# Performance work log

Measured on AMD Instinct MI355X. Metric: run time of the kernel, lower is better.

Reference implementation:

```python
import jax, jax.numpy as jnp
import numpy as np
from jax import lax

B, T = 1024, 1000
EPS = 1e-3  # keras BatchNormalization default epsilon
ALPHA = 0.2  # tf.nn.leaky_relu default alpha


def setup_inputs() -> dict:
    key = jax.random.key(0)
    ks = jax.random.split(key, 40)
    f32 = jnp.float32
    n = lambda k, s, sc=0.1: jax.random.normal(k, s, dtype=f32) * sc
    inp = {"x": jax.random.normal(ks[0], (B, 2, T, 1), dtype=f32)}
    # main conv stack (HWIO kernels)
    inp["c1k"] = n(ks[1], (1, 5, 1, 10));  inp["c1b"] = n(ks[2], (10,), 0.01)
    inp["c2k"] = n(ks[3], (1, 5, 10, 10)); inp["c2b"] = n(ks[4], (10,), 0.01)
    inp["c3k"] = n(ks[5], (1, 5, 10, 10)); inp["c3b"] = n(ks[6], (10,), 0.01)
    inp["c4k"] = n(ks[7], (2, 1, 10, 20)); inp["c4b"] = n(ks[8], (20,), 0.01)
    # batchnorm (inference) params
    for i, k0 in zip((1, 2, 3), (9, 13, 17)):
        inp[f"g{i}"]  = 1.0 + n(ks[k0], (10,), 0.05)
        inp[f"be{i}"] = n(ks[k0 + 1], (10,), 0.05)
        inp[f"m{i}"]  = n(ks[k0 + 2], (10,), 0.05)
        inp[f"v{i}"]  = 1.0 + jax.random.uniform(ks[k0 + 3], (10,), dtype=f32) * 0.1
    # dense head: flatten of [B,1,T-12,20]
    inp["dns_w"] = n(ks[21], ((T - 12) * 20, 1), 0.02)
    inp["dns_b"] = jnp.zeros((1,), f32)
    # MHRSSA blocks: 10 heads of Conv2D(2,(2,1)) stacked -> K [10,2,Cin,2], b [10,2];
    # depthwise (1,5) over 10 channels -> dw [5,10], db [10]
    inp["a1K"] = n(ks[22], (10, 2, 1, 2));  inp["a1b"] = n(ks[23], (10, 2), 0.01)
    inp["a1dw"] = n(ks[24], (5, 10));       inp["a1db"] = n(ks[25], (10,), 0.01)
    inp["a2K"] = n(ks[26], (10, 2, 10, 2)); inp["a2b"] = n(ks[27], (10, 2), 0.01)
    inp["a2dw"] = n(ks[28], (5, 10));       inp["a2db"] = n(ks[29], (10,), 0.01)
    inp["a3K"] = n(ks[30], (10, 2, 10, 2)); inp["a3b"] = n(ks[31], (10, 2), 0.01)
    inp["a3dw"] = n(ks[32], (5, 10));       inp["a3db"] = n(ks[33], (10,), 0.01)
    return inp


def conv2d(x, k, b):
    return lax.conv_general_dilated(x, k, (1, 1), 'VALID',
                                    dimension_numbers=('NHWC', 'HWIO', 'NHWC')) + b


def bn_inf(x, g, be, m, v):
    return (x - m) * (g * lax.rsqrt(v + EPS)) + be


def lrelu(x):
    return jnp.where(x >= 0, x, ALPHA * x)


def mhrssa(x, K, b, dw, db):
    # x: [B,2,T,C]; K: [10,2,C,2] (10 heads of a (2,1)-valid conv) -> [B,10,T,2]
    m = jnp.einsum('bhtc,ihco->bito', x, K) + b[None, :, None, :]
    a = jnp.transpose(m, (0, 3, 2, 1))  # [B,2,T,10]
    Tt = a.shape[2]
    # depthwise (1,5) valid conv over time, per-channel taps dw[w,i]
    y = sum(a[:, :, w:w + Tt - 4, :] * dw[w] for w in range(5)) + db
    return jax.nn.softmax(y, axis=-1)


def reference(x, c1k, c1b, g1, be1, m1, v1, c2k, c2b, g2, be2, m2, v2,
              c3k, c3b, g3, be3, m3, v3, c4k, c4b, dns_w, dns_b,
              a1K, a1b, a1dw, a1db, a2K, a2b, a2dw, a2db, a3K, a3b, a3dw, a3db):
    att1 = mhrssa(x, a1K, a1b, a1dw, a1db)
    h = lrelu(bn_inf(conv2d(x, c1k, c1b), g1, be1, m1, v1)) * att1
    att2 = mhrssa(h, a2K, a2b, a2dw, a2db)
    h = lrelu(bn_inf(conv2d(h, c2k, c2b), g2, be2, m2, v2)) * att2
    att3 = mhrssa(h, a3K, a3b, a3dw, a3db)
    h = lrelu(bn_inf(conv2d(h, c3k, c3b), g3, be3, m3, v3)) * att3
    h = lrelu(conv2d(h, c4k, c4b))          # [B,1,T-12,20]
    h = h.reshape(h.shape[0], -1)
    return h @ dns_w + dns_b                # RGS mode: raw scalar output
```

## Files before the change

### kernel.cpp

```cpp
#include <hip/hip_runtime.h>

#define REP10(X) X(0) X(1) X(2) X(3) X(4) X(5) X(6) X(7) X(8) X(9)
#define REP5(X)  X(0) X(1) X(2) X(3) X(4)

typedef __attribute__((ext_vector_type(2))) float v2;

#define SMX 136

__device__ __forceinline__ void fold_stage(
    float* dst, const float* g, const float* be, const float* mn,
    const float* vr, const float* cb, const float* adw, const float* adb,
    const float* aK, const float* ab, int CIN)
{
  const int tid = threadIdx.x;
  if (tid < 10) {
    const float sc = g[tid] * rsqrtf(vr[tid] + 1e-3f);
    dst[tid]      = sc;
    dst[10 + tid] = (cb[tid] - mn[tid]) * sc + be[tid];
    dst[70 + tid] = adb[tid] * 1.44269504088896340736f;
  }
  if (tid >= 10 && tid < 60)
    dst[10 + tid] = adw[tid - 10] * 1.44269504088896340736f;
  if (tid < 20)
    dst[80 + tid] = ab[(tid % 10) * 2 + tid / 10];
  const int n = 2 * CIN * 2 * 10;
  for (int idx = tid; idx < n; idx += 64) {
    const int i  = idx % 10;
    const int r  = idx / 10;
    const int o  = r % 2;
    const int r2 = r / 2;
    const int ci = r2 % CIN;
    const int h  = r2 / CIN;
    dst[100 + idx] = aK[((i * 2 + h) * CIN + ci) * 2 + o];
  }
}

__global__ void prep_kernel(
    const float* g1, const float* be1, const float* m1, const float* v1,
    const float* cb1, const float* a1dw, const float* a1db,
    const float* a1K, const float* a1b,
    const float* g2, const float* be2, const float* m2, const float* v2_,
    const float* cb2, const float* a2dw, const float* a2db,
    const float* a2K, const float* a2b,
    const float* g3, const float* be3, const float* m3, const float* v3,
    const float* cb3, const float* a3dw, const float* a3db,
    const float* a3K, const float* a3b,
    float* consts)
{
  fold_stage(consts,        g1, be1, m1, v1,  cb1, a1dw, a1db, a1K, a1b, 1);
  fold_stage(consts + 512,  g2, be2, m2, v2_, cb2, a2dw, a2db, a2K, a2b, 10);
  fold_stage(consts + 1024, g3, be3, m3, v3,  cb3, a3dw, a3db, a3K, a3b, 10);
}

template <int CIN>
__global__ __launch_bounds__(128) void stage_kernel(
    const float* __restrict__ in, float* __restrict__ outp, int Tout,
    const float* __restrict__ ck, const float* __restrict__ cst)
{
  __shared__ float smm[5 * SMX * 2];
  const int tid = threadIdx.x;
  const int o   = blockIdx.y;
  const int t0  = blockIdx.x * 128;
  const int Tin = Tout + 4;
  const float* __restrict__ inb =
      in + (size_t)blockIdx.z * (CIN == 1 ? 2000 : 20000);

  const float* __restrict__ scale  = cst;
  const float* __restrict__ shift2 = cst + 10;
  const float* __restrict__ adw2   = cst + 20;
  const float* __restrict__ adb2   = cst + 70;
  const float* __restrict__ abp    = cst + 80;
  const float* __restrict__ aKp    = cst + 100;

  for (int lt = tid; lt < 132; lt += 128) {
    const int t = t0 + lt;
    if (t < Tin) {
#define DECLM(p) v2 mp##p = *reinterpret_cast<const v2*>(abp + o * 10 + 2 * p);
      REP5(DECLM)
#undef DECLM
      if constexpr (CIN == 1) {
#pragma unroll
        for (int h = 0; h < 2; ++h) {
          const float xin = inb[h * 1000 + t];
          const v2 xs = {xin, xin};
          const float* kb = aKp + (h * 2 + o) * 10;
#define FMAM(p) mp##p = __builtin_elementwise_fma(                             \
              xs, *reinterpret_cast<const v2*>(kb + 2 * p), mp##p);
          REP5(FMAM)
#undef FMAM
        }
      } else {
#pragma unroll
        for (int h = 0; h < 2; ++h)
#pragma unroll
          for (int pc = 0; pc < 5; ++pc) {
            const v2 xv = *reinterpret_cast<const v2*>(
                inb + ((pc * 2 + h) * 1000 + t) * 2);
            const v2 xs0 = {xv.x, xv.x};
            const v2 xs1 = {xv.y, xv.y};
            const float* kb0 = aKp + ((h * CIN + 2 * pc) * 2 + o) * 10;
            const float* kb1 = aKp + ((h * CIN + 2 * pc + 1) * 2 + o) * 10;
#define FMAM(p) mp##p = __builtin_elementwise_fma(                             \
                xs0, *reinterpret_cast<const v2*>(kb0 + 2 * p), mp##p);        \
            mp##p = __builtin_elementwise_fma(                                 \
                xs1, *reinterpret_cast<const v2*>(kb1 + 2 * p), mp##p);
            REP5(FMAM)
#undef FMAM
          }
      }
#define STM(p) *reinterpret_cast<v2*>(&smm[(p * SMX + lt) * 2]) = mp##p;
      REP5(STM)
#undef STM
    }
  }
  __syncthreads();

  const int tt = t0 + tid;
  if (tt >= Tout) return;

#define DECLY(p) v2 yp##p = *reinterpret_cast<const v2*>(adb2 + 2 * p);
  REP5(DECLY)
#undef DECLY
#pragma unroll
  for (int w = 0; w < 5; ++w) {
    const float* aw = adw2 + w * 10;
#define FMAY(p) { const v2 sv =                                                \
        *reinterpret_cast<const v2*>(&smm[(p * SMX + tid + w) * 2]);           \
      yp##p = __builtin_elementwise_fma(                                       \
          sv, *reinterpret_cast<const v2*>(aw + 2 * p), yp##p); }
    REP5(FMAY)
#undef FMAY
  }

#define DECLA(p) v2 ap##p = {0.f, 0.f};
  REP5(DECLA)
#undef DECLA
  if constexpr (CIN == 1) {
    const float* __restrict__ cinb = inb + o * 1000 + tt;
#pragma unroll
    for (int w = 0; w < 5; ++w) {
      const float xin = cinb[w];
      const v2 xs = {xin, xin};
      const float* kb = ck + w * 10;
#define FMAC(p) ap##p = __builtin_elementwise_fma(                             \
          xs, *reinterpret_cast<const v2*>(kb + 2 * p), ap##p);
      REP5(FMAC)
#undef FMAC
    }
  } else {
#pragma unroll
    for (int w = 0; w < 5; ++w)
#pragma unroll
      for (int pc = 0; pc < 5; ++pc) {
        const v2 xv = *reinterpret_cast<const v2*>(
            inb + ((pc * 2 + o) * 1000 + tt + w) * 2);
        const v2 xs0 = {xv.x, xv.x};
        const v2 xs1 = {xv.y, xv.y};
        const float* kb0 = ck + (w * CIN + 2 * pc) * 10;
        const float* kb1 = ck + (w * CIN + 2 * pc + 1) * 10;
#define FMAC(p) ap##p = __builtin_elementwise_fma(                             \
            xs0, *reinterpret_cast<const v2*>(kb0 + 2 * p), ap##p);            \
        ap##p = __builtin_elementwise_fma(                                     \
            xs1, *reinterpret_cast<const v2*>(kb1 + 2 * p), ap##p);
        REP5(FMAC)
#undef FMAC
      }
  }

  const float y0 = yp0.x, y1 = yp0.y, y2 = yp1.x, y3 = yp1.y, y4 = yp2.x,
              y5 = yp2.y, y6 = yp3.x, y7 = yp3.y, y8 = yp4.x, y9 = yp4.y;
  float mx = y0;
  mx = fmaxf(mx, y1); mx = fmaxf(mx, y2); mx = fmaxf(mx, y3);
  mx = fmaxf(mx, y4); mx = fmaxf(mx, y5); mx = fmaxf(mx, y6);
  mx = fmaxf(mx, y7); mx = fmaxf(mx, y8); mx = fmaxf(mx, y9);
#define DECLE(i) const float e##i = exp2f(y##i - mx);
  REP10(DECLE)
#undef DECLE
  const float sm  = e0 + e1 + e2 + e3 + e4 + e5 + e6 + e7 + e8 + e9;
  const float inv = __builtin_amdgcn_rcpf(sm);

  float* __restrict__ ob =
      outp + (size_t)blockIdx.z * 20000 + (o * 1000 + tt) * 2;
#define STO(p, ea, eb) {                                                       \
    v2 bv = __builtin_elementwise_fma(                                         \
        ap##p, *reinterpret_cast<const v2*>(scale + 2 * p),                    \
        *reinterpret_cast<const v2*>(shift2 + 2 * p));                         \
    bv = __builtin_elementwise_max(bv, 0.2f * bv);                             \
    const v2 ev = {ea * inv, eb * inv};                                        \
    *reinterpret_cast<v2*>(ob + p * 4000) = bv * ev; }
  STO(0, e0, e1) STO(1, e2, e3) STO(2, e4, e5) STO(3, e6, e7) STO(4, e8, e9)
#undef STO
}

__global__ __launch_bounds__(256) void final_kernel(
    const float* __restrict__ h3, const float* __restrict__ c4k,
    const float* __restrict__ c4b, const float* __restrict__ dnsw,
    const float* __restrict__ dnsb, float* __restrict__ outp, int b0)
{
  __shared__ float red[4];
  const int tid = threadIdx.x;
  const float* __restrict__ hb = h3 + (size_t)blockIdx.x * 20000;
  v2 dotv = {0.f, 0.f};
#pragma unroll 1
  for (int t = tid; t < 988; t += 256) {
#define LDX(p)                                                                 \
    const v2 xa##p = *reinterpret_cast<const v2*>(hb + ((p*2+0)*1000 + t)*2);  \
    const v2 xc##p = *reinterpret_cast<const v2*>(hb + ((p*2+1)*1000 + t)*2);
    REP5(LDX)
#undef LDX
    const float* __restrict__ dwp = dnsw + t * 20;
#pragma unroll
    for (int q = 0; q < 10; ++q) {
      v2 acc = *reinterpret_cast<const v2*>(c4b + 2 * q);
      const float* kq = c4k + 2 * q;
#define FMA4(p) {                                                              \
      const v2 s0 = {xa##p.x, xa##p.x}, s1 = {xa##p.y, xa##p.y};               \
      const v2 s2 = {xc##p.x, xc##p.x}, s3 = {xc##p.y, xc##p.y};               \
      acc = __builtin_elementwise_fma(                                         \
          s0, *reinterpret_cast<const v2*>(kq + (2*p) * 20), acc);             \
      acc = __builtin_elementwise_fma(                                         \
          s1, *reinterpret_cast<const v2*>(kq + (2*p+1) * 20), acc);           \
      acc = __builtin_elementwise_fma(                                         \
          s2, *reinterpret_cast<const v2*>(kq + (10+2*p) * 20), acc);          \
      acc = __builtin_elementwise_fma(                                         \
          s3, *reinterpret_cast<const v2*>(kq + (10+2*p+1) * 20), acc); }
      REP5(FMA4)
#undef FMA4
      acc  = __builtin_elementwise_max(acc, 0.2f * acc);
      dotv = __builtin_elementwise_fma(
          acc, *reinterpret_cast<const v2*>(dwp + 2 * q), dotv);
    }
  }
  float partial = dotv.x + dotv.y;
#pragma unroll
  for (int off = 32; off > 0; off >>= 1)
    partial += __shfl_down(partial, off, 64);
  if ((tid & 63) == 0) red[tid >> 6] = partial;
  __syncthreads();
  if (tid == 0)
    outp[b0 + blockIdx.x] = red[0] + red[1] + red[2] + red[3] + dnsb[0];
}

extern "C" void kernel_launch(void* const* d_in, const int* in_sizes, int n_in,
                              void* d_out, int out_size, void* d_ws, size_t ws_size,
                              hipStream_t stream) {
  const float* p[35];
  for (int i = 0; i < 35; ++i) p[i] = (const float*)d_in[i];
  const int B = in_sizes[0] / 2000;

  float* consts = (float*)d_ws;
  float* hA     = consts + 1536;
  const size_t avail = ws_size - 1536u * 4u;
  int CH = 1024;
  if (CH > B) CH = B;
  while ((size_t)CH * 160000ull > avail && CH > 1) CH >>= 1;
  float* hB = hA + (size_t)CH * 20000;

  prep_kernel<<<dim3(1), dim3(64), 0, stream>>>(
      p[9], p[10], p[11], p[12], p[2], p[25], p[26], p[23], p[24],
      p[13], p[14], p[15], p[16], p[4], p[29], p[30], p[27], p[28],
      p[17], p[18], p[19], p[20], p[6], p[33], p[34], p[31], p[32],
      consts);

  for (int b0 = 0; b0 < B; b0 += CH) {
    const int cc = (B - b0 < CH) ? (B - b0) : CH;
    stage_kernel<1><<<dim3(8, 2, cc), dim3(128), 0, stream>>>(
        p[0] + (size_t)b0 * 2000, hA, 996, p[1], consts);
    stage_kernel<10><<<dim3(8, 2, cc), dim3(128), 0, stream>>>(
        hA, hB, 992, p[3], consts + 512);
    stage_kernel<10><<<dim3(8, 2, cc), dim3(128), 0, stream>>>(
        hB, hA, 988, p[5], consts + 1024);
    final_kernel<<<dim3(cc), dim3(256), 0, stream>>>(
        hA, p[7], p[8], p[21], p[22], (float*)d_out, b0);
  }
}
```

Before: 172.8 us.

## Replace shared-memory halo exchange with wavefront shuffles in stage kernel

The attention pre-activation values are no longer staged through shared memory behind a block barrier. Each 64-lane wavefront now computes 64 time steps, keeps 60 outputs, and reads the 4-step time halo from neighbouring lanes with __shfl_down. Blocks grow to 256 threads (4 wavefronts, 240 outputs per block) and the grid shrinks from 8 to 5 blocks along time. This removes the LDS traffic and __syncthreads, at the cost of about 6% redundant lanes recomputing halo values and many shuffle instructions.

After: 178.4 us. 1.03x slower.

```diff
diff --git a/kernel.cpp b/kernel.cpp
--- a/kernel.cpp
+++ b/kernel.cpp
@@ -4,8 +4,6 @@
 #define REP5(X)  X(0) X(1) X(2) X(3) X(4)
 
 typedef __attribute__((ext_vector_type(2))) float v2;
-
-#define SMX 136
 
 __device__ __forceinline__ void fold_stage(
     float* dst, const float* g, const float* be, const float* mn,
@@ -53,15 +51,18 @@
 }
 
 template <int CIN>
-__global__ __launch_bounds__(128) void stage_kernel(
+__global__ __launch_bounds__(256) void stage_kernel(
     const float* __restrict__ in, float* __restrict__ outp, int Tout,
     const float* __restrict__ ck, const float* __restrict__ cst)
 {
-  __shared__ float smm[5 * SMX * 2];
-  const int tid = threadIdx.x;
-  const int o   = blockIdx.y;
-  const int t0  = blockIdx.x * 128;
-  const int Tin = Tout + 4;
+  const int lane = threadIdx.x & 63;
+  const int wid  = threadIdx.x >> 6;
+  const int o    = blockIdx.y;
+  const int Tin  = Tout + 4;
+  const int t0w  = blockIdx.x * 240 + wid * 60;
+  if (t0w >= Tin) return;
+  const int tm  = t0w + lane;
+  const int tmc = (tm < Tin - 1) ? tm : (Tin - 1);
   const float* __restrict__ inb =
       in + (size_t)blockIdx.z * (CIN == 1 ? 2000 : 20000);
 
@@ -72,65 +73,58 @@
   const float* __restrict__ abp    = cst + 80;
   const float* __restrict__ aKp    = cst + 100;
 
-  for (int lt = tid; lt < 132; lt += 128) {
-    const int t = t0 + lt;
-    if (t < Tin) {
 #define DECLM(p) v2 mp##p = *reinterpret_cast<const v2*>(abp + o * 10 + 2 * p);
-      REP5(DECLM)
+  REP5(DECLM)
 #undef DECLM
-      if constexpr (CIN == 1) {
-#pragma unroll
-        for (int h = 0; h < 2; ++h) {
-          const float xin = inb[h * 1000 + t];
-          const v2 xs = {xin, xin};
-          const float* kb = aKp + (h * 2 + o) * 10;
+  if constexpr (CIN == 1) {
+#pragma unroll
+    for (int h = 0; h < 2; ++h) {
+      const float xin = inb[h * 1000 + tmc];
+      const v2 xs = {xin, xin};
+      const float* kb = aKp + (h * 2 + o) * 10;
 #define FMAM(p) mp##p = __builtin_elementwise_fma(                             \
-              xs, *reinterpret_cast<const v2*>(kb + 2 * p), mp##p);
-          REP5(FMAM)
+          xs, *reinterpret_cast<const v2*>(kb + 2 * p), mp##p);
+      REP5(FMAM)
 #undef FMAM
-        }
-      } else {
-#pragma unroll
-        for (int h = 0; h < 2; ++h)
-#pragma unroll
-          for (int pc = 0; pc < 5; ++pc) {
-            const v2 xv = *reinterpret_cast<const v2*>(
-                inb + ((pc * 2 + h) * 1000 + t) * 2);
-            const v2 xs0 = {xv.x, xv.x};
-            const v2 xs1 = {xv.y, xv.y};
-            const float* kb0 = aKp + ((h * CIN + 2 * pc) * 2 + o) * 10;
-            const float* kb1 = aKp + ((h * CIN + 2 * pc + 1) * 2 + o) * 10;
+    }
+  } else {
+#pragma unroll
+    for (int h = 0; h < 2; ++h)
+#pragma unroll
+      for (int pc = 0; pc < 5; ++pc) {
+        const v2 xv = *reinterpret_cast<const v2*>(
+            inb + ((pc * 2 + h) * 1000 + tmc) * 2);
+        const v2 xs0 = {xv.x, xv.x};
+        const v2 xs1 = {xv.y, xv.y};
+        const float* kb0 = aKp + ((h * CIN + 2 * pc) * 2 + o) * 10;
+        const float* kb1 = aKp + ((h * CIN + 2 * pc + 1) * 2 + o) * 10;
 #define FMAM(p) mp##p = __builtin_elementwise_fma(                             \
-                xs0, *reinterpret_cast<const v2*>(kb0 + 2 * p), mp##p);        \
-            mp##p = __builtin_elementwise_fma(                                 \
-                xs1, *reinterpret_cast<const v2*>(kb1 + 2 * p), mp##p);
-            REP5(FMAM)
+            xs0, *reinterpret_cast<const v2*>(kb0 + 2 * p), mp##p);            \
+        mp##p = __builtin_elementwise_fma(                                     \
+            xs1, *reinterpret_cast<const v2*>(kb1 + 2 * p), mp##p);
+        REP5(FMAM)
 #undef FMAM
-          }
       }
-#define STM(p) *reinterpret_cast<v2*>(&smm[(p * SMX + lt) * 2]) = mp##p;
-      REP5(STM)
-#undef STM
-    }
-  }
-  __syncthreads();
-
-  const int tt = t0 + tid;
-  if (tt >= Tout) return;
-
-#define DECLY(p) v2 yp##p = *reinterpret_cast<const v2*>(adb2 + 2 * p);
+  }
+
+#define DECLY(p) v2 yp##p = __builtin_elementwise_fma(                         \
+      mp##p, *reinterpret_cast<const v2*>(adw2 + 2 * p),                       \
+      *reinterpret_cast<const v2*>(adb2 + 2 * p));
   REP5(DECLY)
 #undef DECLY
 #pragma unroll
-  for (int w = 0; w < 5; ++w) {
-    const float* aw = adw2 + w * 10;
-#define FMAY(p) { const v2 sv =                                                \
-        *reinterpret_cast<const v2*>(&smm[(p * SMX + tid + w) * 2]);           \
+  for (int k = 1; k < 5; ++k) {
+    const float* aw = adw2 + k * 10;
+#define FMAY(p) { const v2 sv = {__shfl_down(mp##p.x, k, 64),                  \
+                                 __shfl_down(mp##p.y, k, 64)};                 \
       yp##p = __builtin_elementwise_fma(                                       \
           sv, *reinterpret_cast<const v2*>(aw + 2 * p), yp##p); }
     REP5(FMAY)
 #undef FMAY
   }
+
+  const int tt = tm;
+  if (lane >= 60 || tt >= Tout) return;
 
 #define DECLA(p) v2 ap##p = {0.f, 0.f};
   REP5(DECLA)
@@ -264,11 +258,11 @@
 
   for (int b0 = 0; b0 < B; b0 += CH) {
     const int cc = (B - b0 < CH) ? (B - b0) : CH;
-    stage_kernel<1><<<dim3(8, 2, cc), dim3(128), 0, stream>>>(
+    stage_kernel<1><<<dim3(5, 2, cc), dim3(256), 0, stream>>>(
         p[0] + (size_t)b0 * 2000, hA, 996, p[1], consts);
-    stage_kernel<10><<<dim3(8, 2, cc), dim3(128), 0, stream>>>(
+    stage_kernel<10><<<dim3(5, 2, cc), dim3(256), 0, stream>>>(
         hA, hB, 992, p[3], consts + 512);
-    stage_kernel<10><<<dim3(8, 2, cc), dim3(128), 0, stream>>>(
+    stage_kernel<10><<<dim3(5, 2, cc), dim3(256), 0, stream>>>(
         hB, hA, 988, p[5], consts + 1024);
     final_kernel<<<dim3(cc), dim3(256), 0, stream>>>(
         hA, p[7], p[8], p[21], p[22], (float*)d_out, b0);
```
